# Kernel optimization log

Hardware: AMD Instinct MI355X
Metric: run time of the kernel (lower is better)

Reference implementation:

```python
import jax, jax.numpy as jnp
import numpy as np

IN_DIM = 128
NUM_IDX = 128
LATENT = 512
FF_HID = 4 * IN_DIM
EPS = 1e-5


def _layernorm(x, g, b):
    mu = jnp.mean(x, axis=-1, keepdims=True)
    var = jnp.mean((x - mu) ** 2, axis=-1, keepdims=True)
    return (x - mu) * jax.lax.rsqrt(var + EPS) * g + b


def setup_inputs() -> dict:
    key = jax.random.key(0)
    ks = jax.random.split(key, 12)
    B, N, D, L = 16, NUM_IDX, IN_DIM, LATENT
    s = lambda fan_in: 1.0 / np.sqrt(fan_in)
    return {
        "in_obs": jax.random.normal(ks[0], (B, N, D), jnp.float32),
        "Wq_w": jax.random.normal(ks[1], (D, L), jnp.float32) * s(D),
        "Wq_b": jax.random.normal(ks[2], (L,), jnp.float32) * s(D),
        "Wk_w": jax.random.normal(ks[3], (D, L), jnp.float32) * s(D),
        "Wk_b": jax.random.normal(ks[4], (L,), jnp.float32) * s(D),
        "wv_w": jax.random.normal(ks[5], (2 * L + 2 * N,), jnp.float32) * s(2 * L + 2 * N),
        "wv_b": jax.random.normal(ks[6], (), jnp.float32) * s(2 * L + 2 * N),
        "g1": jnp.ones((D,), jnp.float32),
        "b1": jnp.zeros((D,), jnp.float32),
        "ff1_w": jax.random.normal(ks[7], (D, FF_HID), jnp.float32) * s(D),
        "ff1_b": jax.random.normal(ks[8], (FF_HID,), jnp.float32) * s(D),
        "ff2_w": jax.random.normal(ks[9], (FF_HID, D), jnp.float32) * s(FF_HID),
        "ff2_b": jax.random.normal(ks[10], (D,), jnp.float32) * s(FF_HID),
        "g2": jnp.ones((D,), jnp.float32),
        "b2": jnp.zeros((D,), jnp.float32),
    }


def reference(in_obs, Wq_w, Wq_b, Wk_w, Wk_b, wv_w, wv_b, g1, b1,
              ff1_w, ff1_b, ff2_w, ff2_b, g2, b2):
    # in_obs: [B, N, D]
    B, N, D = in_obs.shape
    L = Wq_w.shape[1]
    eye = jnp.broadcast_to(jnp.eye(N, dtype=in_obs.dtype), (B, N, N))
    # q_cat/k_cat: [B, N, L+N]
    q_cat = jnp.concatenate([in_obs @ Wq_w + Wq_b, eye], axis=-1)
    k_cat = jnp.concatenate([in_obs @ Wk_w + Wk_b, eye], axis=-1)
    # Original: w_v(tanh(concat(q_i, k_j))). tanh is elementwise and the dot
    # product splits over the concat, so score[b,i,j] = a[b,i] + c[b,j] + bias
    # -- mathematically identical, avoids the [B,N,N,2L+2N] intermediate.
    a = jnp.tanh(q_cat) @ wv_w[: L + N]          # [B, N]
    c = jnp.tanh(k_cat) @ wv_w[L + N:]           # [B, N]
    scores = a[:, :, None] + c[:, None, :] + wv_b  # [B, N, N]
    weights = jax.nn.softmax(scores, axis=-1)
    attn = weights @ in_obs                       # [B, N, D]
    res = _layernorm(attn + in_obs, g1, b1)
    ff = jax.nn.relu(res @ ff1_w + ff1_b) @ ff2_w + ff2_b
    return _layernorm(ff + in_obs, g2, b2)
```

## Files before the change

kernel.cpp:

```cpp
#include <hip/hip_runtime.h>

#define NN 128
#define DD 128
#define LL 512
#define FFH 512
#define TANH1 0.76159415595576489f

typedef __attribute__((ext_vector_type(8))) short bf16x8;
typedef __attribute__((ext_vector_type(4))) float f32x4;

struct alignas(16) f4arr { float v[4]; };

__device__ __forceinline__ unsigned short f2bf(float f) {
    union { float f; unsigned u; } v; v.f = f;
    return (unsigned short)((v.u + 0x7FFFu + ((v.u >> 16) & 1u)) >> 16);
}

__global__ __launch_bounds__(256) void kA(
    const float* __restrict__ in_obs,
    const float* __restrict__ Wk_w,
    const float* __restrict__ Wk_b,
    const float* __restrict__ wv_w,
    const float* __restrict__ ff1_w,
    const float* __restrict__ ff2_w,
    float* __restrict__ c_out,
    unsigned short* __restrict__ W1f,
    unsigned short* __restrict__ W2f)
{
    const int t = threadIdx.x;
    const int wave = t >> 6, lane = t & 63;

    if (blockIdx.x >= 256) {
        const int bi = blockIdx.x - 256;
        const int fg = bi & 127;
        const int jp = t >> 6;
        const int l15 = lane & 15, l4 = lane >> 4;
        const int j = jp * 2;
        unsigned short v0, v1;
        unsigned short* dst;
        if (bi < 128) {
            const int ks = fg & 3, mt = fg >> 2;
            v0 = f2bf(ff1_w[(ks * 32 + l4 * 8 + j    ) * FFH + mt * 16 + l15]);
            v1 = f2bf(ff1_w[(ks * 32 + l4 * 8 + j + 1) * FFH + mt * 16 + l15]);
            dst = W1f;
        } else {
            const int ks = fg & 15, mt = fg >> 4;
            v0 = f2bf(ff2_w[(ks * 32 + l4 * 8 + j    ) * DD + mt * 16 + l15]);
            v1 = f2bf(ff2_w[(ks * 32 + l4 * 8 + j + 1) * DD + mt * 16 + l15]);
            dst = W2f;
        }
        *(unsigned*)&dst[(fg * 64 + lane) * 8 + j] = (unsigned)v0 | ((unsigned)v1 << 16);
        return;
    }

    __shared__ float row_lds[8][128];
    __shared__ float red[8][4];
    const int row0 = blockIdx.x * 8;
    const float* src = in_obs + row0 * DD;
    #pragma unroll
    for (int i = 0; i < 4; ++i) {
        int idx = t + i * 256;
        row_lds[idx >> 7][idx & 127] = src[idx];
    }
    __syncthreads();

    const int l0 = t, l1 = t + 256;
    float acc0[8], acc1[8];
    #pragma unroll
    for (int r = 0; r < 8; ++r) { acc0[r] = 0.f; acc1[r] = 0.f; }

    #pragma unroll 4
    for (int d = 0; d < 128; d += 4) {
        f4arr rbuf[8];
        #pragma unroll
        for (int r = 0; r < 8; ++r)
            rbuf[r] = *(const f4arr*)&row_lds[r][d];
        #pragma unroll
        for (int dd = 0; dd < 4; ++dd) {
            const float w0 = Wk_w[(d + dd) * LL + l0];
            const float w1 = Wk_w[(d + dd) * LL + l1];
            #pragma unroll
            for (int r = 0; r < 8; ++r) {
                acc0[r] += rbuf[r].v[dd] * w0;
                acc1[r] += rbuf[r].v[dd] * w1;
            }
        }
    }
    const float kb0 = Wk_b[l0], kb1 = Wk_b[l1];
    const float wv0 = wv_w[640 + l0], wv1 = wv_w[640 + l1];
    float v[8];
    #pragma unroll
    for (int r = 0; r < 8; ++r)
        v[r] = tanhf(acc0[r] + kb0) * wv0 + tanhf(acc1[r] + kb1) * wv1;
    #pragma unroll
    for (int off = 32; off > 0; off >>= 1) {
        #pragma unroll
        for (int r = 0; r < 8; ++r)
            v[r] += __shfl_down(v[r], off, 64);
    }
    if (lane == 0) {
        #pragma unroll
        for (int r = 0; r < 8; ++r) red[r][wave] = v[r];
    }
    __syncthreads();
    if (t < 8) {
        const int row = row0 + t;
        const int j = row & (NN - 1);
        c_out[row] = red[t][0] + red[t][1] + red[t][2] + red[t][3]
                   + TANH1 * wv_w[1152 + j];
    }
}

__global__ __launch_bounds__(512, 4) void kB(
    const float* __restrict__ in_obs,
    const float* __restrict__ c_in,
    const unsigned short* __restrict__ W1f,
    const unsigned short* __restrict__ W2f,
    const float* __restrict__ g1, const float* __restrict__ b1,
    const float* __restrict__ ff1_b,
    const float* __restrict__ ff2_b,
    const float* __restrict__ g2, const float* __restrict__ b2,
    float* __restrict__ out)
{
    const int t = threadIdx.x;
    const int b = blockIdx.x >> 3;
    const int j0 = (blockIdx.x & 7) * 16;
    const int wave = t >> 6, lane = t & 63;
    const int l15 = lane & 15, l4 = lane >> 4;

    __shared__ float part[8][128];
    __shared__ alignas(16) unsigned short res_lds[16 * 128];
    __shared__ alignas(16) unsigned short h_lds[16 * 512];
    __shared__ alignas(16) float o2_lds[16 * 128];

    const float cv0 = c_in[b * NN + lane];
    const float cv1 = c_in[b * NN + lane + 64];
    float mx = fmaxf(cv0, cv1);
    #pragma unroll
    for (int off = 32; off > 0; off >>= 1) mx = fmaxf(mx, __shfl_xor(mx, off, 64));
    float e0 = __expf(cv0 - mx), e1 = __expf(cv1 - mx);
    float sm = e0 + e1;
    #pragma unroll
    for (int off = 32; off > 0; off >>= 1) sm += __shfl_xor(sm, off, 64);
    const float inv = 1.f / sm;
    e0 *= inv; e1 *= inv;

    {
        const float* base = in_obs + (b * NN + wave * 16) * DD;
        float a0 = 0.f, a1 = 0.f;
        #pragma unroll
        for (int jj = 0; jj < 16; ++jj) {
            const int js = wave * 16 + jj;
            const float wj = (wave < 4) ? __shfl(e0, js, 64)
                                        : __shfl(e1, js - 64, 64);
            a0 += wj * base[jj * DD + lane];
            a1 += wj * base[jj * DD + 64 + lane];
        }
        part[wave][lane] = a0;
        part[wave][lane + 64] = a1;
    }
    __syncthreads();

    {
        const int c0i = lane * 2;
        float a0 = 0.f, a1 = 0.f;
        #pragma unroll
        for (int g = 0; g < 8; ++g) {
            const float2 p = *(const float2*)&part[g][c0i];
            a0 += p.x; a1 += p.y;
        }
        const float2 gv = *(const float2*)&g1[c0i];
        const float2 bv = *(const float2*)&b1[c0i];
        #pragma unroll
        for (int rr = 0; rr < 2; ++rr) {
            const int r = wave + rr * 8;
            const int row = b * NN + j0 + r;
            const float2 xo = *(const float2*)&in_obs[row * DD + c0i];
            const float x0 = a0 + xo.x, x1 = a1 + xo.y;
            float s = x0 + x1;
            #pragma unroll
            for (int off = 32; off > 0; off >>= 1) s += __shfl_xor(s, off, 64);
            const float mu = s * (1.f / 128.f);
            const float d0 = x0 - mu, d1 = x1 - mu;
            float vs = d0 * d0 + d1 * d1;
            #pragma unroll
            for (int off = 32; off > 0; off >>= 1) vs += __shfl_xor(vs, off, 64);
            const float rstd = rsqrtf(vs * (1.f / 128.f) + 1e-5f);
            const float r0 = d0 * rstd * gv.x + bv.x;
            const float r1 = d1 * rstd * gv.y + bv.y;
            const unsigned pk = (unsigned)f2bf(r0) | ((unsigned)f2bf(r1) << 16);
            const int swz = (lane * 4) ^ ((r & 7) << 4);
            *(unsigned*)((char*)res_lds + r * 256 + swz) = pk;
        }
    }
    __syncthreads();

    {
        bf16x8 bfrag[4];
        #pragma unroll
        for (int ks = 0; ks < 4; ++ks) {
            const int off = l15 * 256 + ((ks * 64 + l4 * 16) ^ ((l15 & 7) << 4));
            bfrag[ks] = *(const bf16x8*)((const char*)res_lds + off);
        }
        #pragma unroll
        for (int i = 0; i < 4; ++i) {
            const int mt = wave * 4 + i;
            f32x4 acc = {0.f, 0.f, 0.f, 0.f};
            #pragma unroll
            for (int ks = 0; ks < 4; ++ks) {
                const bf16x8 afrag = *(const bf16x8*)(W1f + ((mt * 4 + ks) * 64 + lane) * 8);
                acc = __builtin_amdgcn_mfma_f32_16x16x32_bf16(afrag, bfrag[ks], acc, 0, 0, 0);
            }
            const f4arr bias = *(const f4arr*)&ff1_b[mt * 16 + l4 * 4];
            uint2 pk;
            pk.x = (unsigned)f2bf(fmaxf(acc[0] + bias.v[0], 0.f))
                 | ((unsigned)f2bf(fmaxf(acc[1] + bias.v[1], 0.f)) << 16);
            pk.y = (unsigned)f2bf(fmaxf(acc[2] + bias.v[2], 0.f))
                 | ((unsigned)f2bf(fmaxf(acc[3] + bias.v[3], 0.f)) << 16);
            const int off = l15 * 1024 + ((mt * 32 + l4 * 8) ^ ((l15 & 7) << 4));
            *(uint2*)((char*)h_lds + off) = pk;
        }
    }
    __syncthreads();

    {
        f32x4 acc = {0.f, 0.f, 0.f, 0.f};
        #pragma unroll
        for (int ks = 0; ks < 16; ++ks) {
            const int off = l15 * 1024 + ((ks * 64 + l4 * 16) ^ ((l15 & 7) << 4));
            const bf16x8 bfrag = *(const bf16x8*)((const char*)h_lds + off);
            const bf16x8 afrag = *(const bf16x8*)(W2f + ((wave * 16 + ks) * 64 + lane) * 8);
            acc = __builtin_amdgcn_mfma_f32_16x16x32_bf16(afrag, bfrag, acc, 0, 0, 0);
        }
        const int off = l15 * 512 + ((wave * 64 + l4 * 16) ^ ((l15 & 7) << 4));
        *(f32x4*)((char*)o2_lds + off) = acc;
    }
    __syncthreads();

    {
        const int c0i = lane * 2;
        const float2 fb = *(const float2*)&ff2_b[c0i];
        const float2 gv = *(const float2*)&g2[c0i];
        const float2 bv = *(const float2*)&b2[c0i];
        #pragma unroll
        for (int rr = 0; rr < 2; ++rr) {
            const int r = wave + rr * 8;
            const int row = b * NN + j0 + r;
            const int off = r * 512 + ((lane * 8) ^ ((r & 7) << 4));
            const float2 o2 = *(const float2*)((char*)o2_lds + off);
            const float2 xo = *(const float2*)&in_obs[row * DD + c0i];
            const float f0 = o2.x + fb.x + xo.x;
            const float f1 = o2.y + fb.y + xo.y;
            float s = f0 + f1;
            #pragma unroll
            for (int off2 = 32; off2 > 0; off2 >>= 1) s += __shfl_xor(s, off2, 64);
            const float mu = s * (1.f / 128.f);
            const float d0 = f0 - mu, d1 = f1 - mu;
            float vs = d0 * d0 + d1 * d1;
            #pragma unroll
            for (int off2 = 32; off2 > 0; off2 >>= 1) vs += __shfl_xor(vs, off2, 64);
            const float rstd = rsqrtf(vs * (1.f / 128.f) + 1e-5f);
            float2 o;
            o.x = d0 * rstd * gv.x + bv.x;
            o.y = d1 * rstd * gv.y + bv.y;
            *(float2*)&out[row * DD + c0i] = o;
        }
    }
}

extern "C" void kernel_launch(void* const* d_in, const int* in_sizes, int n_in,
                              void* d_out, int out_size, void* d_ws, size_t ws_size,
                              hipStream_t stream) {
    const float* in_obs = (const float*)d_in[0];
    const float* Wk_w  = (const float*)d_in[3];
    const float* Wk_b  = (const float*)d_in[4];
    const float* wv_w  = (const float*)d_in[5];
    const float* g1    = (const float*)d_in[7];
    const float* b1    = (const float*)d_in[8];
    const float* ff1_w = (const float*)d_in[9];
    const float* ff1_b = (const float*)d_in[10];
    const float* ff2_w = (const float*)d_in[11];
    const float* ff2_b = (const float*)d_in[12];
    const float* g2    = (const float*)d_in[13];
    const float* b2    = (const float*)d_in[14];
    float* outp = (float*)d_out;

    unsigned short* W1f = (unsigned short*)d_ws;
    unsigned short* W2f = W1f + 65536;
    float* c_ws = (float*)((char*)d_ws + 262144);

    kA<<<512, 256, 0, stream>>>(in_obs, Wk_w, Wk_b, wv_w, ff1_w, ff2_w,
                                c_ws, W1f, W2f);
    kB<<<128, 512, 0, stream>>>(in_obs, c_ws, W1f, W2f, g1, b1,
                                ff1_b, ff2_b, g2, b2, outp);
}
```

Before: 26.17 us.

## Split kB into 4-row blocks across 512 CTAs and add cache-warming kernel

The main fused attention/FFN kernel now assigns 4 output rows per block instead of 16, so it launches 512 blocks rather than 128 and uses more of the GPU's compute units. The 16-row MFMA tiles are padded with zero rows, and waves 4-7 only write zeros into the LDS row buffer. Each block still recomputes the full softmax-weighted sum over its batch. A new kWarm kernel runs before kB and touches in_obs, the packed weights and the small parameter vectors to pull them into cache. The cost is four times the redundant attention work and MFMA work wasted on padding rows, plus one extra kernel launch.

Result: slower. 30.58 us (+16.9%).

```diff
diff --git a/kernel.cpp b/kernel.cpp
--- a/kernel.cpp
+++ b/kernel.cpp
@@ -111,6 +111,42 @@
     }
 }
 
+__global__ __launch_bounds__(512) void kWarm(
+    const float* __restrict__ in_obs,
+    const float* __restrict__ c_in,
+    const unsigned short* __restrict__ W1f,
+    const unsigned short* __restrict__ W2f,
+    const float* __restrict__ g1, const float* __restrict__ b1,
+    const float* __restrict__ ff1_b,
+    const float* __restrict__ ff2_b,
+    const float* __restrict__ g2, const float* __restrict__ b2)
+{
+    const int t = threadIdx.x;
+    const int blk = blockIdx.x;
+    const int b = blk >> 5;
+    float acc = 0.f;
+
+    const float4* iob = (const float4*)(in_obs + b * NN * DD);
+    #pragma unroll
+    for (int i = 0; i < 8; ++i) {
+        const float4 v = iob[t + i * 512];
+        acc += v.x + v.y + v.z + v.w;
+    }
+    const int s = (blk >> 3) & 63;
+    if (t < 128) {
+        const uint4 w1 = ((const uint4*)W1f)[s * 128 + t];
+        acc += (float)(w1.x ^ w1.w);
+    } else if (t < 256) {
+        const uint4 w2 = ((const uint4*)W2f)[s * 128 + (t - 128)];
+        acc += (float)(w2.x ^ w2.w);
+    }
+    acc += c_in[b * NN + (t & 127)];
+    if (t < 128)
+        acc += g1[t] + b1[t] + g2[t] + b2[t] + ff2_b[t];
+    acc += ff1_b[t];
+    asm volatile("" :: "v"(acc));
+}
+
 __global__ __launch_bounds__(512, 4) void kB(
     const float* __restrict__ in_obs,
     const float* __restrict__ c_in,
@@ -123,8 +159,8 @@
     float* __restrict__ out)
 {
     const int t = threadIdx.x;
-    const int b = blockIdx.x >> 3;
-    const int j0 = (blockIdx.x & 7) * 16;
+    const int b = blockIdx.x >> 5;
+    const int j0 = (blockIdx.x & 31) * 4;
     const int wave = t >> 6, lane = t & 63;
     const int l15 = lane & 15, l4 = lane >> 4;
 
@@ -161,36 +197,38 @@
     }
     __syncthreads();
 
-    {
+    if (wave < 4) {
+        const int r = wave;
+        const int row = b * NN + j0 + r;
         const int c0i = lane * 2;
-        float a0 = 0.f, a1 = 0.f;
+        const float2 xo = *(const float2*)&in_obs[row * DD + c0i];
+        float x0 = xo.x, x1 = xo.y;
         #pragma unroll
         for (int g = 0; g < 8; ++g) {
             const float2 p = *(const float2*)&part[g][c0i];
-            a0 += p.x; a1 += p.y;
-        }
+            x0 += p.x; x1 += p.y;
+        }
+        float s = x0 + x1;
+        #pragma unroll
+        for (int off = 32; off > 0; off >>= 1) s += __shfl_xor(s, off, 64);
+        const float mu = s * (1.f / 128.f);
+        const float d0 = x0 - mu, d1 = x1 - mu;
+        float vs = d0 * d0 + d1 * d1;
+        #pragma unroll
+        for (int off = 32; off > 0; off >>= 1) vs += __shfl_xor(vs, off, 64);
+        const float rstd = rsqrtf(vs * (1.f / 128.f) + 1e-5f);
         const float2 gv = *(const float2*)&g1[c0i];
         const float2 bv = *(const float2*)&b1[c0i];
-        #pragma unroll
-        for (int rr = 0; rr < 2; ++rr) {
-            const int r = wave + rr * 8;
-            const int row = b * NN + j0 + r;
-            const float2 xo = *(const float2*)&in_obs[row * DD + c0i];
-            const float x0 = a0 + xo.x, x1 = a1 + xo.y;
-            float s = x0 + x1;
-            #pragma unroll
-            for (int off = 32; off > 0; off >>= 1) s += __shfl_xor(s, off, 64);
-            const float mu = s * (1.f / 128.f);
-            const float d0 = x0 - mu, d1 = x1 - mu;
-            float vs = d0 * d0 + d1 * d1;
-            #pragma unroll
-            for (int off = 32; off > 0; off >>= 1) vs += __shfl_xor(vs, off, 64);
-            const float rstd = rsqrtf(vs * (1.f / 128.f) + 1e-5f);
-            const float r0 = d0 * rstd * gv.x + bv.x;
-            const float r1 = d1 * rstd * gv.y + bv.y;
-            const unsigned pk = (unsigned)f2bf(r0) | ((unsigned)f2bf(r1) << 16);
-            const int swz = (lane * 4) ^ ((r & 7) << 4);
-            *(unsigned*)((char*)res_lds + r * 256 + swz) = pk;
+        const float r0 = d0 * rstd * gv.x + bv.x;
+        const float r1 = d1 * rstd * gv.y + bv.y;
+        const unsigned pk = (unsigned)f2bf(r0) | ((unsigned)f2bf(r1) << 16);
+        const int swz = (lane * 4) ^ ((r & 7) << 4);
+        *(unsigned*)((char*)res_lds + r * 256 + swz) = pk;
+    } else {
+        #pragma unroll
+        for (int k = 0; k < 3; ++k) {
+            const int r = wave + k * 4;
+            *(unsigned*)((char*)res_lds + r * 256 + lane * 4) = 0u;
         }
     }
     __syncthreads();
@@ -237,34 +275,31 @@
     }
     __syncthreads();
 
-    {
+    if (wave < 4) {
+        const int r = wave;
+        const int row = b * NN + j0 + r;
         const int c0i = lane * 2;
+        const int off = r * 512 + ((lane * 8) ^ ((r & 7) << 4));
+        const float2 o2 = *(const float2*)((char*)o2_lds + off);
         const float2 fb = *(const float2*)&ff2_b[c0i];
+        const float2 xo = *(const float2*)&in_obs[row * DD + c0i];
+        const float f0 = o2.x + fb.x + xo.x;
+        const float f1 = o2.y + fb.y + xo.y;
+        float s = f0 + f1;
+        #pragma unroll
+        for (int off2 = 32; off2 > 0; off2 >>= 1) s += __shfl_xor(s, off2, 64);
+        const float mu = s * (1.f / 128.f);
+        const float d0 = f0 - mu, d1 = f1 - mu;
+        float vs = d0 * d0 + d1 * d1;
+        #pragma unroll
+        for (int off2 = 32; off2 > 0; off2 >>= 1) vs += __shfl_xor(vs, off2, 64);
+        const float rstd = rsqrtf(vs * (1.f / 128.f) + 1e-5f);
         const float2 gv = *(const float2*)&g2[c0i];
         const float2 bv = *(const float2*)&b2[c0i];
-        #pragma unroll
-        for (int rr = 0; rr < 2; ++rr) {
-            const int r = wave + rr * 8;
-            const int row = b * NN + j0 + r;
-            const int off = r * 512 + ((lane * 8) ^ ((r & 7) << 4));
-            const float2 o2 = *(const float2*)((char*)o2_lds + off);
-            const float2 xo = *(const float2*)&in_obs[row * DD + c0i];
-            const float f0 = o2.x + fb.x + xo.x;
-            const float f1 = o2.y + fb.y + xo.y;
-            float s = f0 + f1;
-            #pragma unroll
-            for (int off2 = 32; off2 > 0; off2 >>= 1) s += __shfl_xor(s, off2, 64);
-            const float mu = s * (1.f / 128.f);
-            const float d0 = f0 - mu, d1 = f1 - mu;
-            float vs = d0 * d0 + d1 * d1;
-            #pragma unroll
-            for (int off2 = 32; off2 > 0; off2 >>= 1) vs += __shfl_xor(vs, off2, 64);
-            const float rstd = rsqrtf(vs * (1.f / 128.f) + 1e-5f);
-            float2 o;
-            o.x = d0 * rstd * gv.x + bv.x;
-            o.y = d1 * rstd * gv.y + bv.y;
-            *(float2*)&out[row * DD + c0i] = o;
-        }
+        float2 o;
+        o.x = d0 * rstd * gv.x + bv.x;
+        o.y = d1 * rstd * gv.y + bv.y;
+        *(float2*)&out[row * DD + c0i] = o;
     }
 }
 
@@ -291,6 +326,8 @@
 
     kA<<<512, 256, 0, stream>>>(in_obs, Wk_w, Wk_b, wv_w, ff1_w, ff2_w,
                                 c_ws, W1f, W2f);
-    kB<<<128, 512, 0, stream>>>(in_obs, c_ws, W1f, W2f, g1, b1,
+    kWarm<<<512, 512, 0, stream>>>(in_obs, c_ws, W1f, W2f,
+                                   g1, b1, ff1_b, ff2_b, g2, b2);
+    kB<<<512, 512, 0, stream>>>(in_obs, c_ws, W1f, W2f, g1, b1,
                                 ff1_b, ff2_b, g2, b2, outp);
 }
```

## Halve rows per kB block to double grid and prefetch weight fragments

Applied to the files above, without the earlier changes.

Each kB block now handles 8 rows instead of 16, so the grid doubles from 128 to 256 blocks and covers more of the compute units. The MFMA tiles are zero-padded from 8 to 16 rows. All W1/W2 bf16 fragments are loaded into registers at kernel start, so their global-load latency overlaps with the softmax and attention phase. The trade-off is that half of the MFMA work is wasted on padding rows, the per-batch attention sum is recomputed twice as often, and register pressure rises (launch bounds relaxed to 2).

Result: no change. 25.90 us (median of 2 runs) (-1.0%).

```diff
diff --git a/kernel.cpp b/kernel.cpp
--- a/kernel.cpp
+++ b/kernel.cpp
@@ -111,7 +111,7 @@
     }
 }
 
-__global__ __launch_bounds__(512, 4) void kB(
+__global__ __launch_bounds__(512, 2) void kB(
     const float* __restrict__ in_obs,
     const float* __restrict__ c_in,
     const unsigned short* __restrict__ W1f,
@@ -123,8 +123,8 @@
     float* __restrict__ out)
 {
     const int t = threadIdx.x;
-    const int b = blockIdx.x >> 3;
-    const int j0 = (blockIdx.x & 7) * 16;
+    const int b = blockIdx.x >> 4;
+    const int j0 = (blockIdx.x & 15) * 8;
     const int wave = t >> 6, lane = t & 63;
     const int l15 = lane & 15, l4 = lane >> 4;
 
@@ -132,6 +132,18 @@
     __shared__ alignas(16) unsigned short res_lds[16 * 128];
     __shared__ alignas(16) unsigned short h_lds[16 * 512];
     __shared__ alignas(16) float o2_lds[16 * 128];
+
+    bf16x8 a1p[16];
+    #pragma unroll
+    for (int i = 0; i < 4; ++i)
+        #pragma unroll
+        for (int ks = 0; ks < 4; ++ks)
+            a1p[i * 4 + ks] =
+                *(const bf16x8*)(W1f + (((wave * 4 + i) * 4 + ks) * 64 + lane) * 8);
+    bf16x8 a2p[16];
+    #pragma unroll
+    for (int ks = 0; ks < 16; ++ks)
+        a2p[ks] = *(const bf16x8*)(W2f + ((wave * 16 + ks) * 64 + lane) * 8);
 
     const float cv0 = c_in[b * NN + lane];
     const float cv1 = c_in[b * NN + lane + 64];
@@ -162,36 +174,33 @@
     __syncthreads();
 
     {
+        const int r = wave;
+        const int row = b * NN + j0 + r;
         const int c0i = lane * 2;
-        float a0 = 0.f, a1 = 0.f;
+        const float2 xo = *(const float2*)&in_obs[row * DD + c0i];
+        float x0 = xo.x, x1 = xo.y;
         #pragma unroll
         for (int g = 0; g < 8; ++g) {
             const float2 p = *(const float2*)&part[g][c0i];
-            a0 += p.x; a1 += p.y;
-        }
+            x0 += p.x; x1 += p.y;
+        }
+        float s = x0 + x1;
+        #pragma unroll
+        for (int off = 32; off > 0; off >>= 1) s += __shfl_xor(s, off, 64);
+        const float mu = s * (1.f / 128.f);
+        const float d0 = x0 - mu, d1 = x1 - mu;
+        float vs = d0 * d0 + d1 * d1;
+        #pragma unroll
+        for (int off = 32; off > 0; off >>= 1) vs += __shfl_xor(vs, off, 64);
+        const float rstd = rsqrtf(vs * (1.f / 128.f) + 1e-5f);
         const float2 gv = *(const float2*)&g1[c0i];
         const float2 bv = *(const float2*)&b1[c0i];
-        #pragma unroll
-        for (int rr = 0; rr < 2; ++rr) {
-            const int r = wave + rr * 8;
-            const int row = b * NN + j0 + r;
-            const float2 xo = *(const float2*)&in_obs[row * DD + c0i];
-            const float x0 = a0 + xo.x, x1 = a1 + xo.y;
-            float s = x0 + x1;
-            #pragma unroll
-            for (int off = 32; off > 0; off >>= 1) s += __shfl_xor(s, off, 64);
-            const float mu = s * (1.f / 128.f);
-            const float d0 = x0 - mu, d1 = x1 - mu;
-            float vs = d0 * d0 + d1 * d1;
-            #pragma unroll
-            for (int off = 32; off > 0; off >>= 1) vs += __shfl_xor(vs, off, 64);
-            const float rstd = rsqrtf(vs * (1.f / 128.f) + 1e-5f);
-            const float r0 = d0 * rstd * gv.x + bv.x;
-            const float r1 = d1 * rstd * gv.y + bv.y;
-            const unsigned pk = (unsigned)f2bf(r0) | ((unsigned)f2bf(r1) << 16);
-            const int swz = (lane * 4) ^ ((r & 7) << 4);
-            *(unsigned*)((char*)res_lds + r * 256 + swz) = pk;
-        }
+        const float r0 = d0 * rstd * gv.x + bv.x;
+        const float r1 = d1 * rstd * gv.y + bv.y;
+        const unsigned pk = (unsigned)f2bf(r0) | ((unsigned)f2bf(r1) << 16);
+        const int swz = (lane * 4) ^ ((r & 7) << 4);
+        *(unsigned*)((char*)res_lds + r * 256 + swz) = pk;
+        *(unsigned*)((char*)res_lds + (r + 8) * 256 + (lane * 4)) = 0u;
     }
     __syncthreads();
 
@@ -207,10 +216,9 @@
             const int mt = wave * 4 + i;
             f32x4 acc = {0.f, 0.f, 0.f, 0.f};
             #pragma unroll
-            for (int ks = 0; ks < 4; ++ks) {
-                const bf16x8 afrag = *(const bf16x8*)(W1f + ((mt * 4 + ks) * 64 + lane) * 8);
-                acc = __builtin_amdgcn_mfma_f32_16x16x32_bf16(afrag, bfrag[ks], acc, 0, 0, 0);
-            }
+            for (int ks = 0; ks < 4; ++ks)
+                acc = __builtin_amdgcn_mfma_f32_16x16x32_bf16(
+                          a1p[i * 4 + ks], bfrag[ks], acc, 0, 0, 0);
             const f4arr bias = *(const f4arr*)&ff1_b[mt * 16 + l4 * 4];
             uint2 pk;
             pk.x = (unsigned)f2bf(fmaxf(acc[0] + bias.v[0], 0.f))
@@ -229,8 +237,7 @@
         for (int ks = 0; ks < 16; ++ks) {
             const int off = l15 * 1024 + ((ks * 64 + l4 * 16) ^ ((l15 & 7) << 4));
             const bf16x8 bfrag = *(const bf16x8*)((const char*)h_lds + off);
-            const bf16x8 afrag = *(const bf16x8*)(W2f + ((wave * 16 + ks) * 64 + lane) * 8);
-            acc = __builtin_amdgcn_mfma_f32_16x16x32_bf16(afrag, bfrag, acc, 0, 0, 0);
+            acc = __builtin_amdgcn_mfma_f32_16x16x32_bf16(a2p[ks], bfrag, acc, 0, 0, 0);
         }
         const int off = l15 * 512 + ((wave * 64 + l4 * 16) ^ ((l15 & 7) << 4));
         *(f32x4*)((char*)o2_lds + off) = acc;
@@ -238,33 +245,30 @@
     __syncthreads();
 
     {
+        const int r = wave;
+        const int row = b * NN + j0 + r;
         const int c0i = lane * 2;
+        const int off = r * 512 + ((lane * 8) ^ ((r & 7) << 4));
+        const float2 o2 = *(const float2*)((char*)o2_lds + off);
         const float2 fb = *(const float2*)&ff2_b[c0i];
+        const float2 xo = *(const float2*)&in_obs[row * DD + c0i];
+        const float f0 = o2.x + fb.x + xo.x;
+        const float f1 = o2.y + fb.y + xo.y;
+        float s = f0 + f1;
+        #pragma unroll
+        for (int off2 = 32; off2 > 0; off2 >>= 1) s += __shfl_xor(s, off2, 64);
+        const float mu = s * (1.f / 128.f);
+        const float d0 = f0 - mu, d1 = f1 - mu;
+        float vs = d0 * d0 + d1 * d1;
+        #pragma unroll
+        for (int off2 = 32; off2 > 0; off2 >>= 1) vs += __shfl_xor(vs, off2, 64);
+        const float rstd = rsqrtf(vs * (1.f / 128.f) + 1e-5f);
         const float2 gv = *(const float2*)&g2[c0i];
         const float2 bv = *(const float2*)&b2[c0i];
-        #pragma unroll
-        for (int rr = 0; rr < 2; ++rr) {
-            const int r = wave + rr * 8;
-            const int row = b * NN + j0 + r;
-            const int off = r * 512 + ((lane * 8) ^ ((r & 7) << 4));
-            const float2 o2 = *(const float2*)((char*)o2_lds + off);
-            const float2 xo = *(const float2*)&in_obs[row * DD + c0i];
-            const float f0 = o2.x + fb.x + xo.x;
-            const float f1 = o2.y + fb.y + xo.y;
-            float s = f0 + f1;
-            #pragma unroll
-            for (int off2 = 32; off2 > 0; off2 >>= 1) s += __shfl_xor(s, off2, 64);
-            const float mu = s * (1.f / 128.f);
-            const float d0 = f0 - mu, d1 = f1 - mu;
-            float vs = d0 * d0 + d1 * d1;
-            #pragma unroll
-            for (int off2 = 32; off2 > 0; off2 >>= 1) vs += __shfl_xor(vs, off2, 64);
-            const float rstd = rsqrtf(vs * (1.f / 128.f) + 1e-5f);
-            float2 o;
-            o.x = d0 * rstd * gv.x + bv.x;
-            o.y = d1 * rstd * gv.y + bv.y;
-            *(float2*)&out[row * DD + c0i] = o;
-        }
+        float2 o;
+        o.x = d0 * rstd * gv.x + bv.x;
+        o.y = d1 * rstd * gv.y + bv.y;
+        *(float2*)&out[row * DD + c0i] = o;
     }
 }
 
@@ -291,6 +295,6 @@
 
     kA<<<512, 256, 0, stream>>>(in_obs, Wk_w, Wk_b, wv_w, ff1_w, ff2_w,
                                 c_ws, W1f, W2f);
-    kB<<<128, 512, 0, stream>>>(in_obs, c_ws, W1f, W2f, g1, b1,
+    kB<<<256, 512, 0, stream>>>(in_obs, c_ws, W1f, W2f, g1, b1,
                                 ff1_b, ff2_b, g2, b2, outp);
 }
```
